# Optimization experiments

Hardware: AMD Instinct MI355X
Metric: run time of the kernel (lower is better)

## Reference

```python
import jax, jax.numpy as jnp
import numpy as np

N_DRUG = 572
D = 512
K = 64          # neighbor_sample_size
T = 30000       # tail entities
R = 200         # relations
MAX_DEG = 32    # padded invariant_adj neighbor count
EPS = 1e-5


def setup_inputs() -> dict:
    key = jax.random.key(0)
    ks = jax.random.split(key, 10)
    return {
        "drug_embed_W": jax.random.normal(ks[0], (N_DRUG, D), jnp.float32),
        "rela_embed_W": jax.random.normal(ks[1], (R, D), jnp.float32),
        "ent_embed_W": jax.random.normal(ks[2], (T, D), jnp.float32),
        "Wa": jax.random.normal(ks[3], (D, D), jnp.float32) / np.float32(np.sqrt(D)),
        "lin_W": jax.random.normal(ks[4], (2 * D, D), jnp.float32) / np.float32(np.sqrt(2 * D)),
        "lin_b": jnp.zeros((D,), jnp.float32),
        "gamma": jnp.ones((D,), jnp.float32),
        "beta": jnp.zeros((D,), jnp.float32),
        "drug_name": jnp.arange(N_DRUG, dtype=jnp.int64 if jax.config.jax_enable_x64 else jnp.int32),
        "adj_tail": jax.random.randint(ks[5], (N_DRUG, K), 0, T),
        "adj_relation": jax.random.randint(ks[6], (N_DRUG, K), 0, R),
        "nbr_idx": jax.random.randint(ks[7], (N_DRUG, MAX_DEG), 0, N_DRUG),
        "nbr_deg": jax.random.randint(ks[8], (N_DRUG,), 0, MAX_DEG),
        "epoch": 2,
    }


def _forward(drug_embed_W, rela_embed_W, ent_embed_W, Wa, lin_W, lin_b, gamma, beta,
             drug_name, adj_tail, adj_relation, nbr_idx, nbr_deg, epoch):
    drug_e = drug_embed_W[drug_name]          # [N, D]
    rela = rela_embed_W[adj_relation]         # [N, K, D]
    ent = ent_embed_W[adj_tail]               # [N, K, D]

    # relation-aware attention over sampled neighbors (AttentionLayer)
    q = drug_e @ Wa                           # [N, D]
    scores = jnp.einsum('nd,nkd->nk', q, rela) * (1.0 / np.float32(np.sqrt(D)))
    attn = jax.nn.softmax(scores, axis=1)     # [N, K]
    agg = jnp.einsum('nk,nkd->nd', attn, ent) # [N, D]

    # Linear1: Linear(2D->D) + ReLU + BatchNorm1d (training-mode batch stats)
    h = jnp.concatenate([agg, drug_e], axis=1) @ lin_W + lin_b
    h = jax.nn.relu(h)
    mean = jnp.mean(h, axis=0)
    var = jnp.var(h, axis=0)                  # biased, as torch BN normalization
    drug_f = (h - mean) * jax.lax.rsqrt(var + EPS) * gamma + beta

    if epoch > 1:
        # sequential per-node neighbor-mean smoothing (in-place semantics)
        mask = (jnp.arange(MAX_DEG)[None, :] < nbr_deg[:, None])  # [N, MAX_DEG]

        def step(f, i):
            pos = nbr_idx[i]
            m = mask[i][:, None].astype(f.dtype)
            s = jnp.sum(f[pos] * m, axis=0)
            deg = nbr_deg[i]
            avg = s / jnp.maximum(deg, 1).astype(f.dtype)
            new = jnp.where(deg > 0, (avg + f[i]) * 0.5, f[i])
            return f.at[i].set(new), None

        drug_f, _ = jax.lax.scan(step, drug_f, jnp.arange(N_DRUG))
    return drug_f


def reference(drug_embed_W, rela_embed_W, ent_embed_W, Wa, lin_W, lin_b, gamma, beta,
              drug_name, adj_tail, adj_relation, nbr_idx, nbr_deg, epoch):
    return _forward(drug_embed_W, rela_embed_W, ent_embed_W, Wa, lin_W, lin_b, gamma, beta,
                    drug_name, adj_tail, adj_relation, nbr_idx, nbr_deg, epoch)
```

## Files before the change

kernel.cpp:

```cpp
#include <hip/hip_runtime.h>

#define N_DRUG 572
#define DIM 512
#define MAXDEG 32
#define FS 17

__global__ __launch_bounds__(512) void fwd_kernel(
    const float* __restrict__ drugW, const float* __restrict__ relaW,
    const float* __restrict__ entW, const float* __restrict__ Wa,
    const float* __restrict__ linW, const float* __restrict__ linb,
    const int* __restrict__ drug_name, const int* __restrict__ adj_tail,
    const int* __restrict__ adj_rel, float* __restrict__ out)
{
    __shared__ float cin[4][1024];
    __shared__ float red[4][4][512];
    __shared__ float qs[4][512];
    __shared__ float at[4][64];
    __shared__ int   tails[4][64];
    __shared__ int   rels[4][64];

    const int t  = threadIdx.x;
    const int n0 = blockIdx.x * 4;
    const int c4 = (t & 127) * 4;
    const int kh = t >> 7;

    #pragma unroll
    for (int d = 0; d < 4; ++d) {
        const int rd = drug_name[n0 + d];
        cin[d][512 + t] = drugW[(size_t)rd * 512 + t];
    }
    if (t < 256) {
        const int d = t >> 6, kk = t & 63;
        tails[d][kk] = adj_tail[(n0 + d) * 64 + kk];
        rels[d][kk]  = adj_rel[(n0 + d) * 64 + kk];
    }
    __syncthreads();

    {
        float acc[4][4] = {{0.f}};
        const float* wp = Wa + (size_t)(kh * 128) * 512 + c4;
        const int kb = 512 + kh * 128;
        for (int k0 = 0; k0 < 128; k0 += 4) {
            const float4 w0 = *(const float4*)(wp + (size_t)(k0 + 0) * 512);
            const float4 w1 = *(const float4*)(wp + (size_t)(k0 + 1) * 512);
            const float4 w2 = *(const float4*)(wp + (size_t)(k0 + 2) * 512);
            const float4 w3 = *(const float4*)(wp + (size_t)(k0 + 3) * 512);
            const float4 ww[4] = {w0, w1, w2, w3};
            #pragma unroll
            for (int u = 0; u < 4; ++u) {
                const float4 w = ww[u];
                #pragma unroll
                for (int d = 0; d < 4; ++d) {
                    const float b = cin[d][kb + k0 + u];
                    acc[d][0] = fmaf(b, w.x, acc[d][0]);
                    acc[d][1] = fmaf(b, w.y, acc[d][1]);
                    acc[d][2] = fmaf(b, w.z, acc[d][2]);
                    acc[d][3] = fmaf(b, w.w, acc[d][3]);
                }
            }
        }
        #pragma unroll
        for (int d = 0; d < 4; ++d)
            *(float4*)&red[kh][d][c4] = make_float4(acc[d][0], acc[d][1], acc[d][2], acc[d][3]);
    }
    __syncthreads();
    #pragma unroll
    for (int d = 0; d < 4; ++d)
        qs[d][t] = red[0][d][t] + red[1][d][t] + red[2][d][t] + red[3][d][t];
    __syncthreads();

    {
        const int w = t >> 6, lane = t & 63;
        const int d = w >> 1;
        float qv[8];
        {
            const float4* qp = (const float4*)&qs[d][lane * 8];
            const float4 x = qp[0], y = qp[1];
            qv[0]=x.x; qv[1]=x.y; qv[2]=x.z; qv[3]=x.w;
            qv[4]=y.x; qv[5]=y.y; qv[6]=y.z; qv[7]=y.w;
        }
        #pragma unroll 4
        for (int kk = 0; kk < 32; ++kk) {
            const int k = (w & 1) * 32 + kk;
            const float4* p = (const float4*)(relaW + (size_t)rels[d][k] * 512 + lane * 8);
            const float4 x = p[0], y = p[1];
            float s = 0.f;
            s = fmaf(qv[0], x.x, s); s = fmaf(qv[1], x.y, s);
            s = fmaf(qv[2], x.z, s); s = fmaf(qv[3], x.w, s);
            s = fmaf(qv[4], y.x, s); s = fmaf(qv[5], y.y, s);
            s = fmaf(qv[6], y.z, s); s = fmaf(qv[7], y.w, s);
            #pragma unroll
            for (int off = 32; off >= 1; off >>= 1) s += __shfl_xor(s, off, 64);
            if (lane == 0) at[d][k] = s * 0.0441941738241592f;
        }
    }
    __syncthreads();

    {
        const int w = t >> 6, lane = t & 63;
        if ((w & 1) == 0) {
            const int d = w >> 1;
            const float s = at[d][lane];
            float m = s;
            #pragma unroll
            for (int off = 32; off >= 1; off >>= 1) m = fmaxf(m, __shfl_xor(m, off, 64));
            const float e = __expf(s - m);
            float sum = e;
            #pragma unroll
            for (int off = 32; off >= 1; off >>= 1) sum += __shfl_xor(sum, off, 64);
            at[d][lane] = e / sum;
        }
    }
    __syncthreads();

    {
        const int d = t >> 7;
        const int cg = (t & 127) * 4;
        float a0 = 0.f, a1 = 0.f, a2 = 0.f, a3 = 0.f;
        #pragma unroll 8
        for (int k = 0; k < 64; ++k) {
            const float ak = at[d][k];
            const float4 e = *(const float4*)(entW + (size_t)tails[d][k] * 512 + cg);
            a0 = fmaf(ak, e.x, a0); a1 = fmaf(ak, e.y, a1);
            a2 = fmaf(ak, e.z, a2); a3 = fmaf(ak, e.w, a3);
        }
        *(float4*)&cin[d][cg] = make_float4(a0, a1, a2, a3);
    }
    __syncthreads();

    {
        float acc[4][4] = {{0.f}};
        const int kb = kh * 256;
        const float* wp = linW + (size_t)kb * 512 + c4;
        for (int k0 = 0; k0 < 256; k0 += 4) {
            const float4 w0 = *(const float4*)(wp + (size_t)(k0 + 0) * 512);
            const float4 w1 = *(const float4*)(wp + (size_t)(k0 + 1) * 512);
            const float4 w2 = *(const float4*)(wp + (size_t)(k0 + 2) * 512);
            const float4 w3 = *(const float4*)(wp + (size_t)(k0 + 3) * 512);
            const float4 ww[4] = {w0, w1, w2, w3};
            #pragma unroll
            for (int u = 0; u < 4; ++u) {
                const float4 w = ww[u];
                #pragma unroll
                for (int d = 0; d < 4; ++d) {
                    const float b = cin[d][kb + k0 + u];
                    acc[d][0] = fmaf(b, w.x, acc[d][0]);
                    acc[d][1] = fmaf(b, w.y, acc[d][1]);
                    acc[d][2] = fmaf(b, w.z, acc[d][2]);
                    acc[d][3] = fmaf(b, w.w, acc[d][3]);
                }
            }
        }
        #pragma unroll
        for (int d = 0; d < 4; ++d)
            *(float4*)&red[kh][d][c4] = make_float4(acc[d][0], acc[d][1], acc[d][2], acc[d][3]);
    }
    __syncthreads();
    {
        const float bb = linb[t];
        #pragma unroll
        for (int d = 0; d < 4; ++d) {
            const float v = red[0][d][t] + red[1][d][t] + red[2][d][t] + red[3][d][t] + bb;
            out[(size_t)(n0 + d) * 512 + t] = fmaxf(v, 0.f);
        }
    }
}

__global__ __launch_bounds__(512) void scan_kernel(
    float* hout, const float* __restrict__ gamma, const float* __restrict__ beta,
    const int* __restrict__ nbr_idx, const int* __restrict__ nbr_deg,
    const int* __restrict__ epoch)
{
    __shared__ float fs[(N_DRUG + 1) * FS];
    __shared__ alignas(16) unsigned short offs[N_DRUG * MAXDEG];
    __shared__ float2 ivw[N_DRUG];
    __shared__ int   mxs[N_DRUG];
    __shared__ float part[2][32][16];
    __shared__ float bnp[2][16];
    __shared__ int   genext[2];
    __shared__ int   ge0s;

    const int t  = threadIdx.x;
    const int c  = t & 15;
    const int h  = (t >> 4) & 1;
    const int j  = t >> 5;
    const int rr = t >> 4;
    const int c0 = blockIdx.x * 16;

    for (int i = t; i < N_DRUG; i += 512) {
        const int d = nbr_deg[i];
        ivw[i] = (d > 0) ? make_float2(0.5f / (float)d, 0.5f) : make_float2(0.f, 1.f);
        const int4* np = (const int4*)&nbr_idx[i * MAXDEG];
        unsigned* op = (unsigned*)&offs[i * MAXDEG];
        int mx = -1;
        #pragma unroll
        for (int u = 0; u < 8; ++u) {
            int4 qq = np[u];
            const int b = u * 4;
            qq.x = (b + 0 < d) ? qq.x : N_DRUG;
            qq.y = (b + 1 < d) ? qq.y : N_DRUG;
            qq.z = (b + 2 < d) ? qq.z : N_DRUG;
            qq.w = (b + 3 < d) ? qq.w : N_DRUG;
            mx = max(mx, (qq.x < i) ? qq.x : -1);
            mx = max(mx, (qq.y < i) ? qq.y : -1);
            mx = max(mx, (qq.z < i) ? qq.z : -1);
            mx = max(mx, (qq.w < i) ? qq.w : -1);
            op[2 * u]     = (unsigned)(qq.x * FS) | ((unsigned)(qq.y * FS) << 16);
            op[2 * u + 1] = (unsigned)(qq.z * FS) | ((unsigned)(qq.w * FS) << 16);
        }
        mxs[i] = mx;
    }

    {
        float sl = 0.f, ql = 0.f;
        for (int r = rr; r < N_DRUG; r += 32) {
            const float v = hout[(size_t)r * DIM + c0 + c];
            fs[r * FS + c] = v;
            sl += v;
            ql = fmaf(v, v, ql);
        }
        part[0][rr][c] = sl;
        part[1][rr][c] = ql;
    }
    if (t < FS) fs[N_DRUG * FS + t] = 0.f;
    __syncthreads();

    if (t < 16) {
        float s = 0.f, sq = 0.f;
        #pragma unroll
        for (int k = 0; k < 32; ++k) { s += part[0][k][t]; sq += part[1][k][t]; }
        const float mean = s * (1.f / N_DRUG);
        const float var = sq * (1.f / N_DRUG) - mean * mean;
        const float rstd = rsqrtf(var + 1e-5f);
        const float scl = gamma[c0 + t] * rstd;
        bnp[0][t] = scl;
        bnp[1][t] = beta[c0 + t] - mean * scl;
    }
    if ((t >> 6) == 7) {
        const int l = t & 63;
        const int jj = 1 + l;
        const bool flag = (l >= 15) || (jj >= N_DRUG) || (mxs[min(jj, N_DRUG - 1)] >= 0);
        const unsigned long long b = __ballot(flag) & 0xFFFFULL;
        if (l == 0) ge0s = 1 + (int)__builtin_ctzll(b);
    }
    __syncthreads();

    {
        const float scl = bnp[0][c];
        const float shf = bnp[1][c];
        for (int r = rr; r < N_DRUG; r += 32)
            fs[r * FS + c] = fmaf(fs[r * FS + c], scl, shf);
    }
    __syncthreads();

    if (epoch[0] > 1) {
        int gs = 0, ge = ge0s;
        uint4 ca, cb;
        {
            const uint4* p = (const uint4*)&offs[min(j, N_DRUG - 1) * MAXDEG + h * 16];
            ca = p[0]; cb = p[1];
        }
        int par = 0;
        while (gs < N_DRUG) {
            const bool pred = (gs + j) < ge;
            float s0 = 0.f, s1 = 0.f;
#define G2(W) { s0 += fs[(W & 0xffffu) + c]; s1 += fs[(W >> 16) + c]; }
            if (pred) { G2(ca.x) G2(ca.y) G2(ca.z) G2(ca.w)
                        G2(cb.x) G2(cb.y) G2(cb.z) G2(cb.w) }
#undef G2
            uint4 na, nb;
            {
                const uint4* p = (const uint4*)&offs[min(ge + j, N_DRUG - 1) * MAXDEG + h * 16];
                na = p[0]; nb = p[1];
            }
            float nv = 0.f;
            if (pred) {
                const float cur = fs[(gs + j) * FS + c];
                const float2 iw = ivw[gs + j];
                float sh = s0 + s1;
                sh += __shfl_xor(sh, 16, 64);
                nv = fmaf(sh, iw.x, cur * iw.y);
            }
            if ((t >> 6) == 7) {
                const int l = t & 63;
                const int jj = ge + 1 + l;
                const bool flag = (l >= 15) || (jj >= N_DRUG) ||
                                  (mxs[min(jj, N_DRUG - 1)] >= ge);
                const unsigned long long b = __ballot(flag) & 0xFFFFULL;
                if (l == 0) genext[par] = ge + 1 + (int)__builtin_ctzll(b);
            }
            __syncthreads();
            if (pred && h == 0) fs[(gs + j) * FS + c] = nv;
            __syncthreads();
            gs = ge;
            ge = genext[par];
            par ^= 1;
            ca = na; cb = nb;
        }
    }
    __syncthreads();

    for (int r = rr; r < N_DRUG; r += 32)
        hout[(size_t)r * DIM + c0 + c] = fs[r * FS + c];
}

extern "C" void kernel_launch(void* const* d_in, const int* in_sizes, int n_in,
                              void* d_out, int out_size, void* d_ws, size_t ws_size,
                              hipStream_t stream)
{
    const float* drugW = (const float*)d_in[0];
    const float* relaW = (const float*)d_in[1];
    const float* entW  = (const float*)d_in[2];
    const float* Wa    = (const float*)d_in[3];
    const float* linW  = (const float*)d_in[4];
    const float* linb  = (const float*)d_in[5];
    const float* gamma = (const float*)d_in[6];
    const float* beta  = (const float*)d_in[7];
    const int* drug_name = (const int*)d_in[8];
    const int* adj_tail  = (const int*)d_in[9];
    const int* adj_rel   = (const int*)d_in[10];
    const int* nbr_idx   = (const int*)d_in[11];
    const int* nbr_deg   = (const int*)d_in[12];
    const int* epoch     = (const int*)d_in[13];

    float* out = (float*)d_out;

    fwd_kernel<<<N_DRUG / 4, 512, 0, stream>>>(
        drugW, relaW, entW, Wa, linW, linb, drug_name, adj_tail, adj_rel, out);
    scan_kernel<<<32, 512, 0, stream>>>(
        out, gamma, beta, nbr_idx, nbr_deg, epoch);
}
```

Measured before the change: 202.2 us.

## Split fused forward kernel into packed-weight GEMMs and per-drug attention kernel

```diff
diff --git a/kernel.cpp b/kernel.cpp
--- a/kernel.cpp
+++ b/kernel.cpp
@@ -5,165 +5,171 @@
 #define MAXDEG 32
 #define FS 17
 
-__global__ __launch_bounds__(512) void fwd_kernel(
+__global__ __launch_bounds__(256) void pack_both(
+    const float* __restrict__ Wa, const float* __restrict__ linW,
+    float* __restrict__ waP, float* __restrict__ linP)
+{
+    const int g = blockIdx.x * 256 + threadIdx.x;
+    if (g < 65536) {
+        const int c = g & 511, k4 = g >> 9;
+        const float4 v = make_float4(Wa[(size_t)(k4 * 4 + 0) * 512 + c],
+                                     Wa[(size_t)(k4 * 4 + 1) * 512 + c],
+                                     Wa[(size_t)(k4 * 4 + 2) * 512 + c],
+                                     Wa[(size_t)(k4 * 4 + 3) * 512 + c]);
+        *(float4*)&waP[((size_t)(c >> 6) * 128 + k4) * 256 + (c & 63) * 4] = v;
+    } else {
+        const int h = g - 65536;
+        const int c = h & 511, k4 = h >> 9;
+        const float4 v = make_float4(linW[(size_t)(k4 * 4 + 0) * 512 + c],
+                                     linW[(size_t)(k4 * 4 + 1) * 512 + c],
+                                     linW[(size_t)(k4 * 4 + 2) * 512 + c],
+                                     linW[(size_t)(k4 * 4 + 3) * 512 + c]);
+        *(float4*)&linP[((size_t)(c >> 6) * 256 + k4) * 256 + (c & 63) * 4] = v;
+    }
+}
+
+__global__ __launch_bounds__(256) void gemm_q(
+    const float* __restrict__ drugW, const float* __restrict__ waP,
+    const int* __restrict__ dn, float* __restrict__ q)
+{
+    const int wv = threadIdx.x >> 6;
+    const int lane = threadIdx.x & 63;
+    const int r0 = (blockIdx.x * 4 + wv) * 8;
+    const int c = blockIdx.y * 64 + lane;
+
+    const float* ap[8];
+    #pragma unroll
+    for (int r = 0; r < 8; ++r) {
+        const int rr = min(r0 + r, N_DRUG - 1);
+        ap[r] = drugW + (size_t)dn[rr] * 512;
+    }
+    const float* wp = waP + (size_t)blockIdx.y * 128 * 256 + lane * 4;
+
+    float acc[8] = {0.f, 0.f, 0.f, 0.f, 0.f, 0.f, 0.f, 0.f};
+    #pragma unroll 4
+    for (int k4 = 0; k4 < 128; ++k4) {
+        const float4 w = *(const float4*)(wp + (size_t)k4 * 256);
+        const int k = k4 * 4;
+        #pragma unroll
+        for (int r = 0; r < 8; ++r) {
+            const float4 a = *(const float4*)(ap[r] + k);
+            acc[r] = fmaf(a.x, w.x, acc[r]);
+            acc[r] = fmaf(a.y, w.y, acc[r]);
+            acc[r] = fmaf(a.z, w.z, acc[r]);
+            acc[r] = fmaf(a.w, w.w, acc[r]);
+        }
+    }
+    #pragma unroll
+    for (int r = 0; r < 8; ++r)
+        if (r0 + r < N_DRUG) q[(size_t)(r0 + r) * 512 + c] = acc[r];
+}
+
+__global__ __launch_bounds__(256) void attn_kernel(
     const float* __restrict__ drugW, const float* __restrict__ relaW,
-    const float* __restrict__ entW, const float* __restrict__ Wa,
-    const float* __restrict__ linW, const float* __restrict__ linb,
-    const int* __restrict__ drug_name, const int* __restrict__ adj_tail,
-    const int* __restrict__ adj_rel, float* __restrict__ out)
-{
-    __shared__ float cin[4][1024];
-    __shared__ float red[4][4][512];
-    __shared__ float qs[4][512];
-    __shared__ float at[4][64];
-    __shared__ int   tails[4][64];
-    __shared__ int   rels[4][64];
-
-    const int t  = threadIdx.x;
-    const int n0 = blockIdx.x * 4;
-    const int c4 = (t & 127) * 4;
-    const int kh = t >> 7;
-
-    #pragma unroll
-    for (int d = 0; d < 4; ++d) {
-        const int rd = drug_name[n0 + d];
-        cin[d][512 + t] = drugW[(size_t)rd * 512 + t];
-    }
-    if (t < 256) {
-        const int d = t >> 6, kk = t & 63;
-        tails[d][kk] = adj_tail[(n0 + d) * 64 + kk];
-        rels[d][kk]  = adj_rel[(n0 + d) * 64 + kk];
-    }
-    __syncthreads();
-
+    const float* __restrict__ entW, const float* __restrict__ qbuf,
+    const int* __restrict__ dn, const int* __restrict__ adj_tail,
+    const int* __restrict__ adj_rel, float* __restrict__ cat)
+{
+    __shared__ float at[64];
+    __shared__ int tails[64];
+    __shared__ int rels[64];
+    const int d = blockIdx.x;
+    const int t = threadIdx.x;
+    const int w = t >> 6, lane = t & 63;
+
+    if (t < 64) {
+        tails[t] = adj_tail[d * 64 + t];
+        rels[t]  = adj_rel[d * 64 + t];
+    }
+    float qv[8];
     {
-        float acc[4][4] = {{0.f}};
-        const float* wp = Wa + (size_t)(kh * 128) * 512 + c4;
-        const int kb = 512 + kh * 128;
-        for (int k0 = 0; k0 < 128; k0 += 4) {
-            const float4 w0 = *(const float4*)(wp + (size_t)(k0 + 0) * 512);
-            const float4 w1 = *(const float4*)(wp + (size_t)(k0 + 1) * 512);
-            const float4 w2 = *(const float4*)(wp + (size_t)(k0 + 2) * 512);
-            const float4 w3 = *(const float4*)(wp + (size_t)(k0 + 3) * 512);
-            const float4 ww[4] = {w0, w1, w2, w3};
-            #pragma unroll
-            for (int u = 0; u < 4; ++u) {
-                const float4 w = ww[u];
-                #pragma unroll
-                for (int d = 0; d < 4; ++d) {
-                    const float b = cin[d][kb + k0 + u];
-                    acc[d][0] = fmaf(b, w.x, acc[d][0]);
-                    acc[d][1] = fmaf(b, w.y, acc[d][1]);
-                    acc[d][2] = fmaf(b, w.z, acc[d][2]);
-                    acc[d][3] = fmaf(b, w.w, acc[d][3]);
-                }
-            }
-        }
-        #pragma unroll
-        for (int d = 0; d < 4; ++d)
-            *(float4*)&red[kh][d][c4] = make_float4(acc[d][0], acc[d][1], acc[d][2], acc[d][3]);
-    }
-    __syncthreads();
-    #pragma unroll
-    for (int d = 0; d < 4; ++d)
-        qs[d][t] = red[0][d][t] + red[1][d][t] + red[2][d][t] + red[3][d][t];
+        const float4* qp = (const float4*)(qbuf + (size_t)d * 512 + lane * 8);
+        const float4 x = qp[0], y = qp[1];
+        qv[0] = x.x; qv[1] = x.y; qv[2] = x.z; qv[3] = x.w;
+        qv[4] = y.x; qv[5] = y.y; qv[6] = y.z; qv[7] = y.w;
+    }
+    __syncthreads();
+
+    #pragma unroll 4
+    for (int kk = 0; kk < 16; ++kk) {
+        const int k = w * 16 + kk;
+        const float4* p = (const float4*)(relaW + (size_t)rels[k] * 512 + lane * 8);
+        const float4 x = p[0], y = p[1];
+        float s = 0.f;
+        s = fmaf(qv[0], x.x, s); s = fmaf(qv[1], x.y, s);
+        s = fmaf(qv[2], x.z, s); s = fmaf(qv[3], x.w, s);
+        s = fmaf(qv[4], y.x, s); s = fmaf(qv[5], y.y, s);
+        s = fmaf(qv[6], y.z, s); s = fmaf(qv[7], y.w, s);
+        #pragma unroll
+        for (int off = 32; off >= 1; off >>= 1) s += __shfl_xor(s, off, 64);
+        if (lane == 0) at[k] = s * 0.0441941738241592f;
+    }
+    __syncthreads();
+
+    if (w == 0) {
+        const float s = at[lane];
+        float m = s;
+        #pragma unroll
+        for (int off = 32; off >= 1; off >>= 1) m = fmaxf(m, __shfl_xor(m, off, 64));
+        const float e = __expf(s - m);
+        float sum = e;
+        #pragma unroll
+        for (int off = 32; off >= 1; off >>= 1) sum += __shfl_xor(sum, off, 64);
+        at[lane] = e / sum;
+    }
     __syncthreads();
 
     {
-        const int w = t >> 6, lane = t & 63;
-        const int d = w >> 1;
-        float qv[8];
-        {
-            const float4* qp = (const float4*)&qs[d][lane * 8];
-            const float4 x = qp[0], y = qp[1];
-            qv[0]=x.x; qv[1]=x.y; qv[2]=x.z; qv[3]=x.w;
-            qv[4]=y.x; qv[5]=y.y; qv[6]=y.z; qv[7]=y.w;
-        }
-        #pragma unroll 4
-        for (int kk = 0; kk < 32; ++kk) {
-            const int k = (w & 1) * 32 + kk;
-            const float4* p = (const float4*)(relaW + (size_t)rels[d][k] * 512 + lane * 8);
-            const float4 x = p[0], y = p[1];
-            float s = 0.f;
-            s = fmaf(qv[0], x.x, s); s = fmaf(qv[1], x.y, s);
-            s = fmaf(qv[2], x.z, s); s = fmaf(qv[3], x.w, s);
-            s = fmaf(qv[4], y.x, s); s = fmaf(qv[5], y.y, s);
-            s = fmaf(qv[6], y.z, s); s = fmaf(qv[7], y.w, s);
-            #pragma unroll
-            for (int off = 32; off >= 1; off >>= 1) s += __shfl_xor(s, off, 64);
-            if (lane == 0) at[d][k] = s * 0.0441941738241592f;
-        }
-    }
-    __syncthreads();
-
-    {
-        const int w = t >> 6, lane = t & 63;
-        if ((w & 1) == 0) {
-            const int d = w >> 1;
-            const float s = at[d][lane];
-            float m = s;
-            #pragma unroll
-            for (int off = 32; off >= 1; off >>= 1) m = fmaxf(m, __shfl_xor(m, off, 64));
-            const float e = __expf(s - m);
-            float sum = e;
-            #pragma unroll
-            for (int off = 32; off >= 1; off >>= 1) sum += __shfl_xor(sum, off, 64);
-            at[d][lane] = e / sum;
-        }
-    }
-    __syncthreads();
-
-    {
-        const int d = t >> 7;
-        const int cg = (t & 127) * 4;
-        float a0 = 0.f, a1 = 0.f, a2 = 0.f, a3 = 0.f;
+        const int c2 = t * 2;
+        float a0 = 0.f, a1 = 0.f;
         #pragma unroll 8
         for (int k = 0; k < 64; ++k) {
-            const float ak = at[d][k];
-            const float4 e = *(const float4*)(entW + (size_t)tails[d][k] * 512 + cg);
-            a0 = fmaf(ak, e.x, a0); a1 = fmaf(ak, e.y, a1);
-            a2 = fmaf(ak, e.z, a2); a3 = fmaf(ak, e.w, a3);
-        }
-        *(float4*)&cin[d][cg] = make_float4(a0, a1, a2, a3);
-    }
-    __syncthreads();
-
-    {
-        float acc[4][4] = {{0.f}};
-        const int kb = kh * 256;
-        const float* wp = linW + (size_t)kb * 512 + c4;
-        for (int k0 = 0; k0 < 256; k0 += 4) {
-            const float4 w0 = *(const float4*)(wp + (size_t)(k0 + 0) * 512);
-            const float4 w1 = *(const float4*)(wp + (size_t)(k0 + 1) * 512);
-            const float4 w2 = *(const float4*)(wp + (size_t)(k0 + 2) * 512);
-            const float4 w3 = *(const float4*)(wp + (size_t)(k0 + 3) * 512);
-            const float4 ww[4] = {w0, w1, w2, w3};
-            #pragma unroll
-            for (int u = 0; u < 4; ++u) {
-                const float4 w = ww[u];
-                #pragma unroll
-                for (int d = 0; d < 4; ++d) {
-                    const float b = cin[d][kb + k0 + u];
-                    acc[d][0] = fmaf(b, w.x, acc[d][0]);
-                    acc[d][1] = fmaf(b, w.y, acc[d][1]);
-                    acc[d][2] = fmaf(b, w.z, acc[d][2]);
-                    acc[d][3] = fmaf(b, w.w, acc[d][3]);
-                }
-            }
-        }
-        #pragma unroll
-        for (int d = 0; d < 4; ++d)
-            *(float4*)&red[kh][d][c4] = make_float4(acc[d][0], acc[d][1], acc[d][2], acc[d][3]);
-    }
-    __syncthreads();
-    {
-        const float bb = linb[t];
-        #pragma unroll
-        for (int d = 0; d < 4; ++d) {
-            const float v = red[0][d][t] + red[1][d][t] + red[2][d][t] + red[3][d][t] + bb;
-            out[(size_t)(n0 + d) * 512 + t] = fmaxf(v, 0.f);
-        }
-    }
+            const float ak = at[k];
+            const float2 e = *(const float2*)(entW + (size_t)tails[k] * 512 + c2);
+            a0 = fmaf(ak, e.x, a0);
+            a1 = fmaf(ak, e.y, a1);
+        }
+        float* o = cat + (size_t)d * 1024;
+        *(float2*)&o[c2] = make_float2(a0, a1);
+        const float2 de = *(const float2*)(drugW + (size_t)dn[d] * 512 + c2);
+        *(float2*)&o[512 + c2] = de;
+    }
+}
+
+__global__ __launch_bounds__(256) void gemm_h(
+    const float* __restrict__ A, const float* __restrict__ linP,
+    const float* __restrict__ bias, float* __restrict__ out)
+{
+    const int wv = threadIdx.x >> 6;
+    const int lane = threadIdx.x & 63;
+    const int r0 = (blockIdx.x * 4 + wv) * 8;
+    const int c = blockIdx.y * 64 + lane;
+
+    const float* ap[8];
+    #pragma unroll
+    for (int r = 0; r < 8; ++r)
+        ap[r] = A + (size_t)min(r0 + r, N_DRUG - 1) * 1024;
+    const float* wp = linP + (size_t)blockIdx.y * 256 * 256 + lane * 4;
+
+    float acc[8] = {0.f, 0.f, 0.f, 0.f, 0.f, 0.f, 0.f, 0.f};
+    #pragma unroll 4
+    for (int k4 = 0; k4 < 256; ++k4) {
+        const float4 w = *(const float4*)(wp + (size_t)k4 * 256);
+        const int k = k4 * 4;
+        #pragma unroll
+        for (int r = 0; r < 8; ++r) {
+            const float4 a = *(const float4*)(ap[r] + k);
+            acc[r] = fmaf(a.x, w.x, acc[r]);
+            acc[r] = fmaf(a.y, w.y, acc[r]);
+            acc[r] = fmaf(a.z, w.z, acc[r]);
+            acc[r] = fmaf(a.w, w.w, acc[r]);
+        }
+    }
+    const float b = bias[c];
+    #pragma unroll
+    for (int r = 0; r < 8; ++r)
+        if (r0 + r < N_DRUG)
+            out[(size_t)(r0 + r) * 512 + c] = fmaxf(acc[r] + b, 0.f);
 }
 
 __global__ __launch_bounds__(512) void scan_kernel(
@@ -325,8 +331,15 @@
 
     float* out = (float*)d_out;
 
-    fwd_kernel<<<N_DRUG / 4, 512, 0, stream>>>(
-        drugW, relaW, entW, Wa, linW, linb, drug_name, adj_tail, adj_rel, out);
-    scan_kernel<<<32, 512, 0, stream>>>(
-        out, gamma, beta, nbr_idx, nbr_deg, epoch);
-}
+    float* qbuf = (float*)d_ws;
+    float* cat  = (float*)((char*)d_ws + 1171456);
+    float* waP  = (float*)((char*)d_ws + 3514368);
+    float* linP = (float*)((char*)d_ws + 4562944);
+
+    pack_both<<<768, 256, 0, stream>>>(Wa, linW, waP, linP);
+    gemm_q<<<dim3(18, 8), 256, 0, stream>>>(drugW, waP, drug_name, qbuf);
+    attn_kernel<<<N_DRUG, 256, 0, stream>>>(drugW, relaW, entW, qbuf,
+                                            drug_name, adj_tail, adj_rel, cat);
+    gemm_h<<<dim3(18, 8), 256, 0, stream>>>(cat, linP, linb, out);
+    scan_kernel<<<32, 512, 0, stream>>>(out, gamma, beta, nbr_idx, nbr_deg, epoch);
+}
```

After: 295.6 us. +46.2%, slower.
